# Performance work log

Hardware: AMD Instinct MI355X
Metric: run time of the kernel (lower is better)

Reference implementation:

```python
import jax, jax.numpy as jnp
import numpy as np

B, D, K, H, N = 2048, 3, 64, 768, 4096  # batch, tree depth, fanout, hidden, internal nodes


def setup_inputs() -> dict:
    key = jax.random.key(0)
    k1, k2, k3, k4, k5 = jax.random.split(key, 5)
    pooled = jax.random.normal(k1, (B, H), dtype=jnp.float32)
    nodes = jax.random.randint(k2, (B, D), 0, N)            # per-sample fc head ids along the label path
    path = jax.random.randint(k3, (B, D), 0, K)             # per-node CE target (child index)
    W = jax.random.normal(k4, (N, K, H), dtype=jnp.float32) * 0.02  # stacked nn.Linear weights
    b = jax.random.normal(k5, (N, K), dtype=jnp.float32) * 0.02     # stacked nn.Linear biases
    return {"pooled": pooled, "nodes": nodes, "path": path, "W": W, "b": b}


def reference(pooled, nodes, path, W, b):
    # Gather each sample's tiny linear heads along its label path: [B, D, K, H]
    Wg = W[nodes]
    bg = b[nodes]                                            # [B, D, K]
    # Per-sample, per-depth gemv: fc[n](feature) for n in nodes
    logits = jnp.einsum('bdkh,bh->bdk', Wg, pooled) + bg     # [B, D, K]
    # Per-node CrossEntropyLoss against path targets, summed over the path
    lse = jax.nn.logsumexp(logits, axis=-1)                  # [B, D]
    tgt = jnp.take_along_axis(logits, path[..., None], axis=-1)[..., 0]  # [B, D]
    losses = jnp.sum(lse - tgt, axis=-1)                     # [B]
    return losses, logits
```

## Files before the change

### kernel.cpp

```cpp
#include <hip/hip_runtime.h>
#include <hip/hip_bf16.h>

#define BATCH   2048
#define DEPTH   3
#define FANOUT  64
#define HID     768
#define NNODES  4096
#define NPAIRS  (BATCH * DEPTH)
#define CAP     16
#define NTAIL   64

#define WS_COUNT 0
#define WS_OCNT  NNODES
#define WS_LIST  (NNODES + 4)
#define WS_OVFL  (WS_LIST + NNODES * CAP)
#define WS_PART  (WS_OVFL + NPAIRS)
#define WS_ZERO_INTS (NNODES + 4)

__global__ __launch_bounds__(256) void bin_kernel(const int* __restrict__ nodes,
                                                  int* __restrict__ ws) {
    int idx = blockIdx.x * 256 + threadIdx.x;
    if (idx >= NPAIRS) return;
    int n = nodes[idx];
    int pos = atomicAdd(&ws[WS_COUNT + n], 1);
    if (pos < CAP) {
        ws[WS_LIST + n * CAP + pos] = idx;
    } else {
        int op = atomicAdd(&ws[WS_OCNT], 1);
        ws[WS_OVFL + op] = idx;
    }
}

__global__ __launch_bounds__(256) void node_gemm_kernel(
    const float* __restrict__ pooled,
    const float* __restrict__ W,
    const float* __restrict__ bias,
    const int*   __restrict__ nodes,
    const int*   __restrict__ path,
    int*         __restrict__ ws,
    float*       __restrict__ logits)
{
    __shared__ int   s_pairs[CAP];
    __shared__ float s_bias[FANOUT];
    __shared__ float s_pool[8][HID];
    __shared__ float s_log[8][FANOUT];

    const int tid  = threadIdx.x;
    const int wave = tid >> 6;
    const int lane = tid & 63;
    float* part = reinterpret_cast<float*>(ws) + WS_PART;

    int c = 0;
    int n = -1;

    if (blockIdx.x < NNODES) {
        n = blockIdx.x;
        c = ws[WS_COUNT + n];
        if (c == 0) return;
        c = min(c, CAP);
        if (tid < c) s_pairs[tid] = ws[WS_LIST + (size_t)n * CAP + tid];
    } else {
        const int oc = min(ws[WS_OCNT], NPAIRS);
        const int i  = (int)blockIdx.x - NNODES;
        if (i >= oc) return;
        c = 1;
        if (tid == 0) s_pairs[0] = ws[WS_OVFL + i];
        __syncthreads();
        n = nodes[s_pairs[0]];
    }
    if (tid < FANOUT) s_bias[tid] = bias[(size_t)n * FANOUT + tid];
    __syncthreads();

    const float4* w4 = reinterpret_cast<const float4*>(W + (size_t)n * FANOUT * HID);

    for (int base = 0; base < c; base += 8) {
        const int sc = min(c - base, 8);
        const int* pair_chunk = s_pairs + base;

        for (int idx = tid; idx < sc * (HID / 4); idx += 256) {
            int s = idx / (HID / 4);
            int f = idx % (HID / 4);
            int b = pair_chunk[s] / DEPTH;
            reinterpret_cast<float4*>(&s_pool[s][0])[f] =
                reinterpret_cast<const float4*>(pooled + (size_t)b * HID)[f];
        }
        __syncthreads();

#pragma unroll 4
        for (int kk = 0; kk < 16; ++kk) {
            const int k = wave * 16 + kk;
            const float4* wr = w4 + (size_t)k * (HID / 4);
            float4 w0 = wr[lane], w1 = wr[lane + 64], w2 = wr[lane + 128];
            for (int s = 0; s < sc; ++s) {
                const float4* a4 = reinterpret_cast<const float4*>(&s_pool[s][0]);
                float4 a0 = a4[lane], a1 = a4[lane + 64], a2 = a4[lane + 128];
                float acc = w0.x * a0.x + w0.y * a0.y + w0.z * a0.z + w0.w * a0.w
                          + w1.x * a1.x + w1.y * a1.y + w1.z * a1.z + w1.w * a1.w
                          + w2.x * a2.x + w2.y * a2.y + w2.z * a2.z + w2.w * a2.w;
#pragma unroll
                for (int off = 32; off > 0; off >>= 1)
                    acc += __shfl_xor(acc, off, 64);
                if (lane == 0) s_log[s][k] = acc + s_bias[k];
            }
        }
        __syncthreads();

        for (int idx = tid; idx < sc * FANOUT; idx += 256) {
            int s = idx >> 6, k = idx & 63;
            logits[(size_t)pair_chunk[s] * FANOUT + k] = s_log[s][k];
        }

        for (int s = wave; s < sc; s += 4) {
            int pair = pair_chunk[s];
            float x = s_log[s][lane];
            float m = x;
#pragma unroll
            for (int off = 32; off > 0; off >>= 1)
                m = fmaxf(m, __shfl_xor(m, off, 64));
            float e = expf(x - m);
#pragma unroll
            for (int off = 32; off > 0; off >>= 1)
                e += __shfl_xor(e, off, 64);
            if (lane == 0) {
                int t = path[pair];
                part[pair] = m + logf(e) - s_log[s][t];
            }
        }
        __syncthreads();
    }
}

__global__ __launch_bounds__(256) void loss_sum_kernel(const int* __restrict__ ws,
                                                       float* __restrict__ losses) {
    const float* part = reinterpret_cast<const float*>(ws) + WS_PART;
    int b = blockIdx.x * 256 + threadIdx.x;
    if (b < BATCH)
        losses[b] = part[b * 3 + 0] + part[b * 3 + 1] + part[b * 3 + 2];
}

extern "C" void kernel_launch(void* const* d_in, const int* in_sizes, int n_in,
                              void* d_out, int out_size, void* d_ws, size_t ws_size,
                              hipStream_t stream) {
    const float* pooled = (const float*)d_in[0];
    const int*   nodes  = (const int*)d_in[1];
    const int*   path   = (const int*)d_in[2];
    const float* W      = (const float*)d_in[3];
    const float* bias   = (const float*)d_in[4];

    float* losses = (float*)d_out;
    float* logits = (float*)d_out + BATCH;
    int*   ws     = (int*)d_ws;

    hipMemsetAsync(ws, 0, WS_ZERO_INTS * sizeof(int), stream);
    hipLaunchKernelGGL(bin_kernel, dim3((NPAIRS + 255) / 256), dim3(256),
                       0, stream, nodes, ws);
    hipLaunchKernelGGL(node_gemm_kernel, dim3(NNODES + NTAIL), dim3(256),
                       0, stream, pooled, W, bias, nodes, path, ws, logits);
    hipLaunchKernelGGL(loss_sum_kernel, dim3((BATCH + 255) / 256), dim3(256),
                       0, stream, ws, losses);
}
```

Before: 139.7 us.

## Split node heads across two blocks and move loss into separate kernel

The node GEMM grid doubles so that each block handles half of a node's 64 output rows. Inside a block, each wave processes 16-lane row groups with templated sample-count accumulators and an SCHUNK of 4. Overflow samples are now handled by strided persistent tail blocks. The logsumexp/CE step moves to a dedicated loss kernel that reads logits back from global memory, which buys more parallelism and occupancy at the cost of an extra logits read and duplicate pooled loads per half.

Result: slower. 411.9 us (+194.8%).

```diff
diff --git a/kernel.cpp b/kernel.cpp
--- a/kernel.cpp
+++ b/kernel.cpp
@@ -9,12 +9,12 @@
 #define NPAIRS  (BATCH * DEPTH)
 #define CAP     16
 #define NTAIL   64
+#define SCHUNK  4
 
 #define WS_COUNT 0
 #define WS_OCNT  NNODES
 #define WS_LIST  (NNODES + 4)
 #define WS_OVFL  (WS_LIST + NNODES * CAP)
-#define WS_PART  (WS_OVFL + NPAIRS)
 #define WS_ZERO_INTS (NNODES + 4)
 
 __global__ __launch_bounds__(256) void bin_kernel(const int* __restrict__ nodes,
@@ -31,111 +31,163 @@
     }
 }
 
-__global__ __launch_bounds__(256) void node_gemm_kernel(
+template <int SC>
+__device__ __forceinline__ void compute_passes(
+    const float4* __restrict__ w4,
+    const float (*s_pool)[HID],
+    float (*s_log)[32],
+    const float* s_bias,
+    int wave, int lane)
+{
+    const int sub = lane & 15;
+    const int rg  = lane >> 4;
+#pragma unroll 1
+    for (int pass = 0; pass < 2; ++pass) {
+        const int kl = wave * 8 + pass * 4 + rg;
+        const float4* wr = w4 + (size_t)kl * (HID / 4);
+        float acc[SC];
+#pragma unroll
+        for (int s = 0; s < SC; ++s) acc[s] = 0.f;
+#pragma unroll
+        for (int it = 0; it < 12; ++it) {
+            float4 w = wr[sub + 16 * it];
+#pragma unroll
+            for (int s = 0; s < SC; ++s) {
+                float4 a = reinterpret_cast<const float4*>(&s_pool[s][0])[sub + 16 * it];
+                acc[s] += w.x * a.x + w.y * a.y + w.z * a.z + w.w * a.w;
+            }
+        }
+#pragma unroll
+        for (int s = 0; s < SC; ++s) {
+            float v = acc[s];
+            v += __shfl_xor(v, 1, 64);
+            v += __shfl_xor(v, 2, 64);
+            v += __shfl_xor(v, 4, 64);
+            v += __shfl_xor(v, 8, 64);
+            if (sub == 0) s_log[s][kl] = v + s_bias[kl];
+        }
+    }
+}
+
+__global__ __launch_bounds__(256, 6) void node_gemm_kernel(
     const float* __restrict__ pooled,
     const float* __restrict__ W,
     const float* __restrict__ bias,
     const int*   __restrict__ nodes,
-    const int*   __restrict__ path,
     int*         __restrict__ ws,
     float*       __restrict__ logits)
 {
     __shared__ int   s_pairs[CAP];
-    __shared__ float s_bias[FANOUT];
-    __shared__ float s_pool[8][HID];
-    __shared__ float s_log[8][FANOUT];
+    __shared__ float s_bias[32];
+    __shared__ float s_pool[SCHUNK][HID];
+    __shared__ float s_log[SCHUNK][32];
 
     const int tid  = threadIdx.x;
     const int wave = tid >> 6;
     const int lane = tid & 63;
-    float* part = reinterpret_cast<float*>(ws) + WS_PART;
-
-    int c = 0;
-    int n = -1;
-
-    if (blockIdx.x < NNODES) {
-        n = blockIdx.x;
-        c = ws[WS_COUNT + n];
+
+    int n, kh, c;
+    int ovfl_stride = 0, ovfl_i = 0, oc = 0;
+
+    if (blockIdx.x < 2 * NNODES) {
+        n  = blockIdx.x & (NNODES - 1);
+        kh = blockIdx.x >> 12;
+        c  = ws[WS_COUNT + n];
         if (c == 0) return;
         c = min(c, CAP);
         if (tid < c) s_pairs[tid] = ws[WS_LIST + (size_t)n * CAP + tid];
     } else {
-        const int oc = min(ws[WS_OCNT], NPAIRS);
-        const int i  = (int)blockIdx.x - NNODES;
-        if (i >= oc) return;
-        c = 1;
-        if (tid == 0) s_pairs[0] = ws[WS_OVFL + i];
+        const int t = (int)blockIdx.x - 2 * NNODES;
+        oc = min(ws[WS_OCNT], NPAIRS);
+        kh = t & 1;
+        ovfl_i = t >> 1;
+        ovfl_stride = NTAIL >> 1;
+        if (ovfl_i >= oc) return;
+        c = -1;
+    }
+
+    if (c > 0) {
+        if (tid < 32) s_bias[tid] = bias[(size_t)n * FANOUT + kh * 32 + tid];
         __syncthreads();
-        n = nodes[s_pairs[0]];
-    }
-    if (tid < FANOUT) s_bias[tid] = bias[(size_t)n * FANOUT + tid];
-    __syncthreads();
-
-    const float4* w4 = reinterpret_cast<const float4*>(W + (size_t)n * FANOUT * HID);
-
-    for (int base = 0; base < c; base += 8) {
-        const int sc = min(c - base, 8);
-        const int* pair_chunk = s_pairs + base;
-
-        for (int idx = tid; idx < sc * (HID / 4); idx += 256) {
-            int s = idx / (HID / 4);
-            int f = idx % (HID / 4);
-            int b = pair_chunk[s] / DEPTH;
-            reinterpret_cast<float4*>(&s_pool[s][0])[f] =
-                reinterpret_cast<const float4*>(pooled + (size_t)b * HID)[f];
-        }
-        __syncthreads();
-
-#pragma unroll 4
-        for (int kk = 0; kk < 16; ++kk) {
-            const int k = wave * 16 + kk;
-            const float4* wr = w4 + (size_t)k * (HID / 4);
-            float4 w0 = wr[lane], w1 = wr[lane + 64], w2 = wr[lane + 128];
-            for (int s = 0; s < sc; ++s) {
-                const float4* a4 = reinterpret_cast<const float4*>(&s_pool[s][0]);
-                float4 a0 = a4[lane], a1 = a4[lane + 64], a2 = a4[lane + 128];
-                float acc = w0.x * a0.x + w0.y * a0.y + w0.z * a0.z + w0.w * a0.w
-                          + w1.x * a1.x + w1.y * a1.y + w1.z * a1.z + w1.w * a1.w
-                          + w2.x * a2.x + w2.y * a2.y + w2.z * a2.z + w2.w * a2.w;
-#pragma unroll
-                for (int off = 32; off > 0; off >>= 1)
-                    acc += __shfl_xor(acc, off, 64);
-                if (lane == 0) s_log[s][k] = acc + s_bias[k];
-            }
-        }
-        __syncthreads();
-
-        for (int idx = tid; idx < sc * FANOUT; idx += 256) {
-            int s = idx >> 6, k = idx & 63;
-            logits[(size_t)pair_chunk[s] * FANOUT + k] = s_log[s][k];
-        }
-
-        for (int s = wave; s < sc; s += 4) {
-            int pair = pair_chunk[s];
-            float x = s_log[s][lane];
-            float m = x;
-#pragma unroll
-            for (int off = 32; off > 0; off >>= 1)
-                m = fmaxf(m, __shfl_xor(m, off, 64));
-            float e = expf(x - m);
-#pragma unroll
-            for (int off = 32; off > 0; off >>= 1)
-                e += __shfl_xor(e, off, 64);
-            if (lane == 0) {
-                int t = path[pair];
-                part[pair] = m + logf(e) - s_log[s][t];
-            }
-        }
-        __syncthreads();
-    }
-}
-
-__global__ __launch_bounds__(256) void loss_sum_kernel(const int* __restrict__ ws,
-                                                       float* __restrict__ losses) {
-    const float* part = reinterpret_cast<const float*>(ws) + WS_PART;
-    int b = blockIdx.x * 256 + threadIdx.x;
-    if (b < BATCH)
-        losses[b] = part[b * 3 + 0] + part[b * 3 + 1] + part[b * 3 + 2];
+        const float4* w4 = reinterpret_cast<const float4*>(
+            W + ((size_t)n * FANOUT + kh * 32) * HID);
+
+        for (int base = 0; base < c; base += SCHUNK) {
+            const int sc = min(c - base, SCHUNK);
+            const int* pair_chunk = s_pairs + base;
+
+            for (int idx = tid; idx < sc * (HID / 4); idx += 256) {
+                int s = idx / (HID / 4), f = idx % (HID / 4);
+                int b = pair_chunk[s] / DEPTH;
+                reinterpret_cast<float4*>(&s_pool[s][0])[f] =
+                    reinterpret_cast<const float4*>(pooled + (size_t)b * HID)[f];
+            }
+            __syncthreads();
+
+            switch (sc) {
+            case 1: compute_passes<1>(w4, s_pool, s_log, s_bias, wave, lane); break;
+            case 2: compute_passes<2>(w4, s_pool, s_log, s_bias, wave, lane); break;
+            case 3: compute_passes<3>(w4, s_pool, s_log, s_bias, wave, lane); break;
+            default: compute_passes<4>(w4, s_pool, s_log, s_bias, wave, lane); break;
+            }
+            __syncthreads();
+
+            for (int idx = tid; idx < sc * 32; idx += 256) {
+                int s = idx >> 5, kl = idx & 31;
+                logits[(size_t)pair_chunk[s] * FANOUT + kh * 32 + kl] = s_log[s][kl];
+            }
+            __syncthreads();
+        }
+    } else {
+        for (int i = ovfl_i; i < oc; i += ovfl_stride) {
+            if (tid == 0) s_pairs[0] = ws[WS_OVFL + i];
+            __syncthreads();
+            const int pair = s_pairs[0];
+            const int nn = nodes[pair];
+            if (tid < 32) s_bias[tid] = bias[(size_t)nn * FANOUT + kh * 32 + tid];
+            const int b = pair / DEPTH;
+            for (int f = tid; f < HID / 4; f += 256)
+                reinterpret_cast<float4*>(&s_pool[0][0])[f] =
+                    reinterpret_cast<const float4*>(pooled + (size_t)b * HID)[f];
+            __syncthreads();
+            const float4* w4 = reinterpret_cast<const float4*>(
+                W + ((size_t)nn * FANOUT + kh * 32) * HID);
+            compute_passes<1>(w4, s_pool, s_log, s_bias, wave, lane);
+            __syncthreads();
+            if (tid < 32)
+                logits[(size_t)pair * FANOUT + kh * 32 + tid] = s_log[0][tid];
+            __syncthreads();
+        }
+    }
+}
+
+__global__ __launch_bounds__(256) void loss_kernel(
+    const float* __restrict__ logits,
+    const int*   __restrict__ path,
+    float*       __restrict__ losses)
+{
+    const int wave = threadIdx.x >> 6;
+    const int lane = threadIdx.x & 63;
+    const int b = blockIdx.x * 4 + wave;
+    if (b >= BATCH) return;
+    const float* lg = logits + (size_t)b * DEPTH * FANOUT;
+    float loss = 0.f;
+#pragma unroll
+    for (int d = 0; d < DEPTH; ++d) {
+        float x = lg[d * FANOUT + lane];
+        float m = x;
+#pragma unroll
+        for (int off = 32; off > 0; off >>= 1)
+            m = fmaxf(m, __shfl_xor(m, off, 64));
+        float e = expf(x - m);
+#pragma unroll
+        for (int off = 32; off > 0; off >>= 1)
+            e += __shfl_xor(e, off, 64);
+        float lse = m + logf(e);
+        int t = path[b * DEPTH + d];
+        loss += lse - __shfl(x, t, 64);
+    }
+    if (lane == 0) losses[b] = loss;
 }
 
 extern "C" void kernel_launch(void* const* d_in, const int* in_sizes, int n_in,
@@ -154,8 +206,8 @@
     hipMemsetAsync(ws, 0, WS_ZERO_INTS * sizeof(int), stream);
     hipLaunchKernelGGL(bin_kernel, dim3((NPAIRS + 255) / 256), dim3(256),
                        0, stream, nodes, ws);
-    hipLaunchKernelGGL(node_gemm_kernel, dim3(NNODES + NTAIL), dim3(256),
-                       0, stream, pooled, W, bias, nodes, path, ws, logits);
-    hipLaunchKernelGGL(loss_sum_kernel, dim3((BATCH + 255) / 256), dim3(256),
-                       0, stream, ws, losses);
-}
+    hipLaunchKernelGGL(node_gemm_kernel, dim3(2 * NNODES + NTAIL), dim3(256),
+                       0, stream, pooled, W, bias, nodes, ws, logits);
+    hipLaunchKernelGGL(loss_kernel, dim3((BATCH + 3) / 4), dim3(256),
+                       0, stream, logits, path, losses);
+}
```

## Template-unroll per-node sample loop and move cross-entropy into separate loss kernel

Applied to the files above, without the earlier changes.

The per-node GEMV inner loop over samples becomes a compile-time-unrolled template (1-4 samples), so the butterfly shuffle reductions of several samples are interleaved instead of serialized. The sample chunk size is reduced from 8 to 4 to match. The logsumexp/target computation moves out of the gemm kernel into a new loss kernel that reads logits back and computes the per-sample loss with one wave per sample, removing the partial-loss workspace. This trades a re-read of logits for a shorter gemm critical path and a smaller shared-memory footprint.

After: 134.9 us. -3.5%, faster.

```diff
diff --git a/kernel.cpp b/kernel.cpp
--- a/kernel.cpp
+++ b/kernel.cpp
@@ -9,12 +9,12 @@
 #define NPAIRS  (BATCH * DEPTH)
 #define CAP     16
 #define NTAIL   64
+#define SCHUNK  4
 
 #define WS_COUNT 0
 #define WS_OCNT  NNODES
 #define WS_LIST  (NNODES + 4)
 #define WS_OVFL  (WS_LIST + NNODES * CAP)
-#define WS_PART  (WS_OVFL + NPAIRS)
 #define WS_ZERO_INTS (NNODES + 4)
 
 __global__ __launch_bounds__(256) void bin_kernel(const int* __restrict__ nodes,
@@ -31,24 +31,58 @@
     }
 }
 
+template <int SC>
+__device__ __forceinline__ void compute_rows(
+    const float4* __restrict__ w4,
+    const float (*s_pool)[HID],
+    float (*s_log)[FANOUT],
+    const float* s_bias,
+    int wave, int lane)
+{
+#pragma unroll 4
+    for (int kk = 0; kk < 16; ++kk) {
+        const int k = wave * 16 + kk;
+        const float4* wr = w4 + (size_t)k * (HID / 4);
+        float4 w0 = wr[lane], w1 = wr[lane + 64], w2 = wr[lane + 128];
+        float v[SC];
+#pragma unroll
+        for (int s = 0; s < SC; ++s) {
+            const float4* a4 = reinterpret_cast<const float4*>(&s_pool[s][0]);
+            float4 a0 = a4[lane], a1 = a4[lane + 64], a2 = a4[lane + 128];
+            v[s] = w0.x * a0.x + w0.y * a0.y + w0.z * a0.z + w0.w * a0.w
+                 + w1.x * a1.x + w1.y * a1.y + w1.z * a1.z + w1.w * a1.w
+                 + w2.x * a2.x + w2.y * a2.y + w2.z * a2.z + w2.w * a2.w;
+        }
+#pragma unroll
+        for (int off = 32; off > 0; off >>= 1) {
+#pragma unroll
+            for (int s = 0; s < SC; ++s)
+                v[s] += __shfl_xor(v[s], off, 64);
+        }
+        if (lane == 0) {
+#pragma unroll
+            for (int s = 0; s < SC; ++s)
+                s_log[s][k] = v[s] + s_bias[k];
+        }
+    }
+}
+
 __global__ __launch_bounds__(256) void node_gemm_kernel(
     const float* __restrict__ pooled,
     const float* __restrict__ W,
     const float* __restrict__ bias,
     const int*   __restrict__ nodes,
-    const int*   __restrict__ path,
     int*         __restrict__ ws,
     float*       __restrict__ logits)
 {
     __shared__ int   s_pairs[CAP];
     __shared__ float s_bias[FANOUT];
-    __shared__ float s_pool[8][HID];
-    __shared__ float s_log[8][FANOUT];
+    __shared__ float s_pool[SCHUNK][HID];
+    __shared__ float s_log[SCHUNK][FANOUT];
 
     const int tid  = threadIdx.x;
     const int wave = tid >> 6;
     const int lane = tid & 63;
-    float* part = reinterpret_cast<float*>(ws) + WS_PART;
 
     int c = 0;
     int n = -1;
@@ -73,8 +107,8 @@
 
     const float4* w4 = reinterpret_cast<const float4*>(W + (size_t)n * FANOUT * HID);
 
-    for (int base = 0; base < c; base += 8) {
-        const int sc = min(c - base, 8);
+    for (int base = 0; base < c; base += SCHUNK) {
+        const int sc = min(c - base, SCHUNK);
         const int* pair_chunk = s_pairs + base;
 
         for (int idx = tid; idx < sc * (HID / 4); idx += 256) {
@@ -86,22 +120,11 @@
         }
         __syncthreads();
 
-#pragma unroll 4
-        for (int kk = 0; kk < 16; ++kk) {
-            const int k = wave * 16 + kk;
-            const float4* wr = w4 + (size_t)k * (HID / 4);
-            float4 w0 = wr[lane], w1 = wr[lane + 64], w2 = wr[lane + 128];
-            for (int s = 0; s < sc; ++s) {
-                const float4* a4 = reinterpret_cast<const float4*>(&s_pool[s][0]);
-                float4 a0 = a4[lane], a1 = a4[lane + 64], a2 = a4[lane + 128];
-                float acc = w0.x * a0.x + w0.y * a0.y + w0.z * a0.z + w0.w * a0.w
-                          + w1.x * a1.x + w1.y * a1.y + w1.z * a1.z + w1.w * a1.w
-                          + w2.x * a2.x + w2.y * a2.y + w2.z * a2.z + w2.w * a2.w;
-#pragma unroll
-                for (int off = 32; off > 0; off >>= 1)
-                    acc += __shfl_xor(acc, off, 64);
-                if (lane == 0) s_log[s][k] = acc + s_bias[k];
-            }
+        switch (sc) {
+        case 1: compute_rows<1>(w4, s_pool, s_log, s_bias, wave, lane); break;
+        case 2: compute_rows<2>(w4, s_pool, s_log, s_bias, wave, lane); break;
+        case 3: compute_rows<3>(w4, s_pool, s_log, s_bias, wave, lane); break;
+        default: compute_rows<4>(w4, s_pool, s_log, s_bias, wave, lane); break;
         }
         __syncthreads();
 
@@ -109,33 +132,37 @@
             int s = idx >> 6, k = idx & 63;
             logits[(size_t)pair_chunk[s] * FANOUT + k] = s_log[s][k];
         }
-
-        for (int s = wave; s < sc; s += 4) {
-            int pair = pair_chunk[s];
-            float x = s_log[s][lane];
-            float m = x;
-#pragma unroll
-            for (int off = 32; off > 0; off >>= 1)
-                m = fmaxf(m, __shfl_xor(m, off, 64));
-            float e = expf(x - m);
-#pragma unroll
-            for (int off = 32; off > 0; off >>= 1)
-                e += __shfl_xor(e, off, 64);
-            if (lane == 0) {
-                int t = path[pair];
-                part[pair] = m + logf(e) - s_log[s][t];
-            }
-        }
         __syncthreads();
     }
 }
 
-__global__ __launch_bounds__(256) void loss_sum_kernel(const int* __restrict__ ws,
-                                                       float* __restrict__ losses) {
-    const float* part = reinterpret_cast<const float*>(ws) + WS_PART;
-    int b = blockIdx.x * 256 + threadIdx.x;
-    if (b < BATCH)
-        losses[b] = part[b * 3 + 0] + part[b * 3 + 1] + part[b * 3 + 2];
+__global__ __launch_bounds__(256) void loss_kernel(
+    const float* __restrict__ logits,
+    const int*   __restrict__ path,
+    float*       __restrict__ losses)
+{
+    const int wave = threadIdx.x >> 6;
+    const int lane = threadIdx.x & 63;
+    const int b = blockIdx.x * 4 + wave;
+    if (b >= BATCH) return;
+    const float* lg = logits + (size_t)b * DEPTH * FANOUT;
+    float loss = 0.f;
+#pragma unroll
+    for (int d = 0; d < DEPTH; ++d) {
+        float x = lg[d * FANOUT + lane];
+        float m = x;
+#pragma unroll
+        for (int off = 32; off > 0; off >>= 1)
+            m = fmaxf(m, __shfl_xor(m, off, 64));
+        float e = expf(x - m);
+#pragma unroll
+        for (int off = 32; off > 0; off >>= 1)
+            e += __shfl_xor(e, off, 64);
+        float lse = m + logf(e);
+        int t = path[b * DEPTH + d];
+        loss += lse - __shfl(x, t, 64);
+    }
+    if (lane == 0) losses[b] = loss;
 }
 
 extern "C" void kernel_launch(void* const* d_in, const int* in_sizes, int n_in,
@@ -155,7 +182,7 @@
     hipLaunchKernelGGL(bin_kernel, dim3((NPAIRS + 255) / 256), dim3(256),
                        0, stream, nodes, ws);
     hipLaunchKernelGGL(node_gemm_kernel, dim3(NNODES + NTAIL), dim3(256),
-                       0, stream, pooled, W, bias, nodes, path, ws, logits);
-    hipLaunchKernelGGL(loss_sum_kernel, dim3((BATCH + 255) / 256), dim3(256),
-                       0, stream, ws, losses);
+                       0, stream, pooled, W, bias, nodes, ws, logits);
+    hipLaunchKernelGGL(loss_kernel, dim3((BATCH + 3) / 4), dim3(256),
+                       0, stream, logits, path, losses);
 }
```
